# Performance work log

Measured on AMD Instinct MI355X. Metric: run time of the kernel, lower is better.

Reference implementation:

```python
import jax, jax.numpy as jnp
import numpy as np
import math

B, N, FEAT, H, NONGT, M, POS = 16, 1024, 768, 8, 20, 10, 64
DG = FEAT // H  # per-head dim = 96
NEG = -9e15


def setup_inputs() -> dict:
    key = jax.random.key(0)
    ks = jax.random.split(key, 14)
    s = 0.02
    return dict(
        roi_feat=jax.random.normal(ks[0], (B, N, FEAT), jnp.float32),
        adj_matrix=jax.random.randint(ks[1], (B, N, NONGT), 0, 2).astype(jnp.int32),
        position_embedding=jax.random.uniform(ks[2], (B, N, NONGT, POS), jnp.float32),
        label_biases_att=jax.random.normal(ks[3], (B, N, NONGT), jnp.float32) * 0.1,
        aux_feat=jax.random.normal(ks[4], (B, 1, FEAT), jnp.float32),
        Wq=jax.random.normal(ks[5], (FEAT, FEAT), jnp.float32) * s,
        bq=jnp.zeros((FEAT,), jnp.float32),
        Wk=jax.random.normal(ks[6], (FEAT, FEAT), jnp.float32) * s,
        bk=jnp.zeros((FEAT,), jnp.float32),
        Wpos=jax.random.normal(ks[7], (POS, H), jnp.float32) * s,
        bpos=jnp.zeros((H,), jnp.float32),
        m_k=jax.random.normal(ks[8], (1, M, FEAT), jnp.float32) * (1.0 / FEAT / H),
        m_v=jax.random.normal(ks[9], (1, M, FEAT), jnp.float32) * (1.0 / M),
        Wout=jax.random.normal(ks[10], (H, DG, FEAT), jnp.float32) * s,  # grouped 1x1 conv: per-head [DG, FEAT]
        bout=jnp.zeros((FEAT,), jnp.float32),
    )


def reference(roi_feat, adj_matrix, position_embedding, label_biases_att, aux_feat,
              Wq, bq, Wk, bk, Wpos, bpos, m_k, m_v, Wout, bout):
    b, n, f = roi_feat.shape
    nongt = min(NONGT, n)
    nongt_feat = roi_feat[:, :nongt]                               # [B,nongt,F]

    q = (roi_feat @ Wq + bq).reshape(b, n, H, DG)                  # [B,N,H,DG]
    scale_m = math.sqrt(f / H)
    mk = scale_m * m_k * aux_feat                                  # [B,M,F] (broadcast)
    mv = scale_m * m_v * aux_feat                                  # [B,M,F]
    k = jnp.concatenate([nongt_feat @ Wk + bk, mk], axis=1)        # [B,K,F], K=nongt+M
    v = jnp.concatenate([nongt_feat, mv], axis=1)                  # [B,K,F]
    kk = k.reshape(b, nongt + M, H, DG)

    # scaled QK^T -> [B,N,H,K]
    aff = jnp.einsum('bnhd,bkhd->bnhk', q, kk) / math.sqrt(DG)

    # geometric position bias: log(max(relu(fc(pos)), 1e-6)) on first nongt keys
    pos = jax.nn.relu(position_embedding @ Wpos + bpos)            # [B,N,nongt,H]
    bias = jnp.log(jnp.maximum(pos, 1e-6))
    aff_n = aff[:, :, :, :nongt] + jnp.transpose(bias, (0, 1, 3, 2))

    # adjacency mask + label bias on first nongt keys
    mask = (adj_matrix > 0)[:, :, None, :]                         # [B,N,1,nongt]
    aff_n = jnp.where(mask, aff_n, NEG) + label_biases_att[:, :, None, :]

    weighted = jnp.concatenate([aff_n, aff[:, :, :, nongt:]], axis=-1)
    p = jax.nn.softmax(weighted, axis=-1)                          # [B,N,H,K]

    out_t = jnp.einsum('bnhk,bkf->bnhf', p, v)                     # [B,N,H,F]
    # weight-normed grouped 1x1 conv == per-head linear F -> DG, concat over heads
    out = jnp.einsum('bnhf,hgf->bnhg', out_t, Wout).reshape(b, n, f) + bout
    return out
```

## Files before the change

kernel.cpp:

```cpp
#include <hip/hip_runtime.h>
#include <hip/hip_bf16.h>
#include <cstdint>

typedef __bf16 bf16;
typedef __bf16 bf16x4 __attribute__((ext_vector_type(4)));
typedef __bf16 bf16x8 __attribute__((ext_vector_type(8)));
typedef float f32x4 __attribute__((ext_vector_type(4)));

#define B_ 16
#define N_ 1024
#define FEAT_ 768
#define H_ 8
#define NONGT_ 20
#define M_ 10
#define POS_ 64
#define DG_ 96
#define KTOT_ 30
#define KPAD_ 32
#define ROWS_ (B_*N_)
#define SCALE_M 9.797958971132712f
#define INV_SQRT_DG 0.10206207261596575f
#define NEG_ -9.0e15f

__device__ __forceinline__ void gload16(const void* g, void* lds) {
  __builtin_amdgcn_global_load_lds(
      (const __attribute__((address_space(1))) unsigned int*)g,
      (__attribute__((address_space(3))) unsigned int*)lds, 16, 0, 0);
}

__device__ __forceinline__ bf16x8 cvt8(float4 a, float4 b) {
  bf16x8 o;
  o[0]=(bf16)a.x; o[1]=(bf16)a.y; o[2]=(bf16)a.z; o[3]=(bf16)a.w;
  o[4]=(bf16)b.x; o[5]=(bf16)b.y; o[6]=(bf16)b.z; o[7]=(bf16)b.w;
  return o;
}

__global__ void prep_kernel(const float* __restrict__ Wq, const float* __restrict__ Wk,
                            const float* __restrict__ Wout, const float* __restrict__ roi,
                            const float* __restrict__ aux, const float* __restrict__ m_v,
                            const float* __restrict__ m_k,
                            bf16* __restrict__ Wq_t, bf16* __restrict__ Wk_t,
                            bf16* __restrict__ Whi, bf16* __restrict__ Wlo,
                            bf16* __restrict__ Vbf, bf16* __restrict__ kbuf,
                            bf16* __restrict__ Abf)
{
  int idx = blockIdx.x * blockDim.x + threadIdx.x;
  int stride = gridDim.x * blockDim.x;
  for (int i = idx; i < FEAT_*FEAT_; i += stride) {
    int k = i / FEAT_, n = i % FEAT_;
    int ksw = (k & ~31) | (((((k >> 3) & 3) ^ ((n >> 1) & 3))) << 3) | (k & 7);
    Wq_t[(size_t)n*FEAT_ + ksw] = (bf16)Wq[i];
    Wk_t[(size_t)n*FEAT_ + k]   = (bf16)Wk[i];
    float w = Wout[i];
    bf16 hi = (bf16)w;
    Whi[i] = hi;
    Wlo[i] = (bf16)(w - (float)hi);
  }
  for (int i = idx; i < B_*KPAD_*FEAT_; i += stride) {
    int f = i % FEAT_;
    int r = (i / FEAT_) % KPAD_;
    int b = i / (FEAT_*KPAD_);
    float v;
    if (r < NONGT_)      v = roi[((size_t)b*N_ + r)*FEAT_ + f];
    else if (r < KTOT_)  v = SCALE_M * m_v[(r-NONGT_)*FEAT_ + f] * aux[b*FEAT_ + f];
    else                 v = 0.f;
    Vbf[i] = (bf16)v;
  }
  for (int i = idx; i < B_*12*FEAT_; i += stride) {
    int f = i % FEAT_;
    int rr = (i / FEAT_) % 12;
    int b = i / (FEAT_*12);
    float v = (rr < M_) ? SCALE_M * m_k[rr*FEAT_ + f] * aux[b*FEAT_ + f] : 0.f;
    kbuf[((size_t)b*KPAD_ + NONGT_ + rr)*FEAT_ + f] = (bf16)v;
  }
  const int total8 = ROWS_*FEAT_/8;
  for (int i = idx; i < total8; i += stride) {
    int row = i / (FEAT_/8);
    int col = (i % (FEAT_/8)) * 8;
    int slot_sw = ((col >> 3) & 3) ^ ((row >> 1) & 3);
    const float4* p = (const float4*)(roi + (size_t)i*8);
    *(bf16x8*)(Abf + (size_t)row*FEAT_ + (col & ~31) + slot_sw*8) = cvt8(p[0], p[1]);
  }
}

__global__ __launch_bounds__(256, 8) void posbias_kernel(
    const float* __restrict__ pe, const float* __restrict__ Wpos,
    const float* __restrict__ bpos, float* __restrict__ posb)
{
  __shared__ __align__(16) float sW[POS_*H_];
  __shared__ float sbp[H_];
  const int tid = threadIdx.x;
  sW[tid] = Wpos[tid];
  sW[256 + tid] = Wpos[256 + tid];
  if (tid < H_) sbp[tid] = bpos[tid];
  __syncthreads();
  const size_t g = (size_t)blockIdx.x*256 + tid;
  const float4* per = (const float4*)(pe + g*POS_);
  double acc[8];
  #pragma unroll
  for (int h = 0; h < 8; ++h) acc[h] = (double)sbp[h];
  #pragma unroll
  for (int p4 = 0; p4 < 16; ++p4) {
    float4 a = per[p4];
    float av[4] = {a.x, a.y, a.z, a.w};
    #pragma unroll
    for (int e = 0; e < 4; ++e) {
      const double ad = (double)av[e];
      const float* wp = sW + (p4*4 + e)*8;
      #pragma unroll
      for (int h = 0; h < 8; ++h)
        acc[h] = fma(ad, (double)wp[h], acc[h]);
    }
  }
  float o[8];
  #pragma unroll
  for (int h = 0; h < 8; ++h) {
    float x = (float)acc[h];
    o[h] = __logf(fmaxf(fmaxf(x, 0.f), 1e-6f));
  }
  float4* po = (float4*)(posb + g*8);
  po[0] = (float4){o[0], o[1], o[2], o[3]};
  po[1] = (float4){o[4], o[5], o[6], o[7]};
}

__global__ __launch_bounds__(256, 2) void gemm_fused_kernel(
    const bf16* __restrict__ Abf, const float* __restrict__ roi,
    const bf16* __restrict__ Wq_t,
    const float* __restrict__ bq, bf16* __restrict__ qbuf,
    const bf16* __restrict__ Wk_t, const bf16* __restrict__ Vbf,
    const bf16* __restrict__ Whi, const bf16* __restrict__ Wlo,
    const float* __restrict__ bk, bf16* __restrict__ kbuf,
    bf16* __restrict__ vwT_hi, bf16* __restrict__ vwT_lo)
{
  __shared__ __align__(16) bf16 sA[128*32];
  __shared__ __align__(16) bf16 sB[128*32];
  const int tid = threadIdx.x;
  const int w = tid >> 6, l = tid & 63;
  const int bx = blockIdx.x;
  const int fr = l & 15, fq = l >> 4, fko = fq << 3;

  if (bx < 768) {
    const int x = bx & 7, j = bx >> 3;
    const int mbase = (x + 8*(j/6)) * 128;
    const int nbase = (j % 6) * 128;
    const int wr = w >> 1, wc = w & 1;
    const int srow = tid >> 2;
    const int scol = (tid & 3) << 3;
    const bf16* Ag0 = Abf + (size_t)(mbase + srow)*FEAT_ + scol;
    const bf16* Ag1 = Ag0 + (size_t)64*FEAT_;
    const bf16* Bg0 = Wq_t + (size_t)(nbase + srow)*FEAT_ + scol;
    const bf16* Bg1 = Bg0 + (size_t)64*FEAT_;
    bf16* ldsA0 = sA + w*512;
    bf16* ldsA1 = sA + 2048 + w*512;
    bf16* ldsB0 = sB + w*512;
    bf16* ldsB1 = sB + 2048 + w*512;
    const int fko_sw = ((fq ^ ((fr >> 1) & 3)) << 3);
    f32x4 acc[4][4] = {};
    for (int kt = 0; kt < FEAT_/32; ++kt) {
      __syncthreads();
      gload16(Ag0 + kt*32, ldsA0);
      gload16(Ag1 + kt*32, ldsA1);
      gload16(Bg0 + kt*32, ldsB0);
      gload16(Bg1 + kt*32, ldsB1);
      __syncthreads();
      bf16x8 af[4], bff[4];
      #pragma unroll
      for (int m = 0; m < 4; ++m)
        af[m] = *(const bf16x8*)(sA + (wr*64 + m*16 + fr)*32 + fko_sw);
      #pragma unroll
      for (int n = 0; n < 4; ++n)
        bff[n] = *(const bf16x8*)(sB + (wc*64 + n*16 + fr)*32 + fko_sw);
      #pragma unroll
      for (int m = 0; m < 4; ++m) {
        #pragma unroll
        for (int n = 0; n < 4; ++n)
          acc[m][n] = __builtin_amdgcn_mfma_f32_16x16x32_bf16(af[m], bff[n], acc[m][n], 0, 0, 0);
      }
    }
    #pragma unroll
    for (int n = 0; n < 4; ++n) {
      const int col = nbase + wc*64 + n*16 + fr;
      const float bv = bq[col];
      #pragma unroll
      for (int m = 0; m < 4; ++m) {
        const int row = mbase + wr*64 + m*16 + fq*4;
        #pragma unroll
        for (int r = 0; r < 4; ++r)
          qbuf[(size_t)(row + r)*FEAT_ + col] = (bf16)(acc[m][n][r] + bv);
      }
    }
  } else {
    const int widx = (bx - 768)*4 + w;
    const int cbase = (widx % 48) * 16;
    const int by = widx / 48;
    f32x4 acc = {};
    if (by < 32) {
      const float* Ap = roi + ((size_t)(by >> 1)*N_ + (by & 1)*16 + fr)*FEAT_ + fko;
      const bf16* Bp = Wk_t + (size_t)(cbase + fr)*FEAT_ + fko;
      #pragma unroll
      for (int kt = 0; kt < FEAT_/32; ++kt) {
        float4 a0 = *(const float4*)(Ap + kt*32);
        float4 a1 = *(const float4*)(Ap + kt*32 + 4);
        bf16x8 b = *(const bf16x8*)(Bp + kt*32);
        acc = __builtin_amdgcn_mfma_f32_16x16x32_bf16(cvt8(a0, a1), b, acc, 0, 0, 0);
      }
      const float bv = bk[cbase + fr];
      #pragma unroll
      for (int r = 0; r < 4; ++r) {
        const int rl = (by & 1)*16 + fq*4 + r;
        if (rl < NONGT_)
          kbuf[((size_t)(by >> 1)*KPAD_ + rl)*FEAT_ + cbase + fr] = (bf16)(acc[r] + bv);
      }
    } else {
      const int rt = by - 32;
      const bf16* Ap = Vbf + ((size_t)rt*16 + fr)*FEAT_ + fko;
      const bf16* B1 = Whi + (size_t)(cbase + fr)*FEAT_ + fko;
      const bf16* B2 = Wlo + (size_t)(cbase + fr)*FEAT_ + fko;
      f32x4 acc2 = {};
      #pragma unroll
      for (int kt = 0; kt < FEAT_/32; ++kt) {
        bf16x8 a = *(const bf16x8*)(Ap + kt*32);
        acc  = __builtin_amdgcn_mfma_f32_16x16x32_bf16(a, *(const bf16x8*)(B1 + kt*32), acc,  0, 0, 0);
        acc2 = __builtin_amdgcn_mfma_f32_16x16x32_bf16(a, *(const bf16x8*)(B2 + kt*32), acc2, 0, 0, 0);
      }
      #pragma unroll
      for (int r = 0; r < 4; ++r) {
        const int grow = rt*16 + fq*4 + r;
        const int b = grow >> 5, key = grow & 31;
        float vv = acc[r] + acc2[r];
        bf16 vh = (bf16)vv;
        size_t addr = ((size_t)b*FEAT_ + cbase + fr)*KPAD_ + key;
        vwT_hi[addr] = vh;
        vwT_lo[addr] = (bf16)(vv - (float)vh);
      }
    }
  }
}

__global__ __launch_bounds__(256, 4) void attn_kernel(
    const bf16* __restrict__ qbuf, const bf16* __restrict__ kbuf,
    const bf16* __restrict__ vwT_hi, const bf16* __restrict__ vwT_lo,
    const float* __restrict__ posb, const int* __restrict__ adj,
    const float* __restrict__ lb, const float* __restrict__ bout,
    float* __restrict__ out)
{
  __shared__ __align__(16) bf16 sph[H_*16*40];
  __shared__ __align__(16) bf16 spl[H_*16*40];
  const int tid = threadIdx.x;
  const int w = tid >> 6, l = tid & 63;
  const int fr = l & 15, fq = l >> 4, fko = fq << 3;
  const int row0 = blockIdx.x * 16;
  const int b = blockIdx.y;
  const size_t rabs = (size_t)b*N_ + row0 + fr;

  #pragma unroll
  for (int hi2 = 0; hi2 < 2; ++hi2) {
    const int h = w*2 + hi2;
    const bf16* kp = kbuf + (size_t)b*KPAD_*FEAT_ + h*DG_ + fko;
    const bf16* qp = qbuf + rabs*FEAT_ + h*DG_ + fko;
    f32x4 acc0 = {}, acc1 = {};
    #pragma unroll
    for (int kt = 0; kt < 3; ++kt) {
      bf16x8 qa = *(const bf16x8*)(qp + kt*32);
      bf16x8 k0 = *(const bf16x8*)(kp + (size_t)fr*FEAT_ + kt*32);
      bf16x8 k1 = *(const bf16x8*)(kp + (size_t)(16 + fr)*FEAT_ + kt*32);
      acc0 = __builtin_amdgcn_mfma_f32_16x16x32_bf16(k0, qa, acc0, 0, 0, 0);
      acc1 = __builtin_amdgcn_mfma_f32_16x16x32_bf16(k1, qa, acc1, 0, 0, 0);
    }
    const float* pbr = posb + rabs*160;
    const int*   adjr = adj + rabs*20;
    const float* lbr  = lb  + rabs*20;
    float lg[2][4];
    #pragma unroll
    for (int r = 0; r < 4; ++r) {
      int j0 = fq*4 + r;
      float v0 = acc0[r] * INV_SQRT_DG;
      v0 = (adjr[j0] > 0 ? v0 + pbr[j0*8 + h] : NEG_) + lbr[j0];
      lg[0][r] = v0;
      int j1 = 16 + fq*4 + r;
      float v1 = acc1[r] * INV_SQRT_DG;
      if (j1 < NONGT_)      v1 = (adjr[j1] > 0 ? v1 + pbr[j1*8 + h] : NEG_) + lbr[j1];
      else if (j1 >= KTOT_) v1 = -3.0e38f;
      lg[1][r] = v1;
    }
    float m = lg[0][0];
    #pragma unroll
    for (int jt = 0; jt < 2; ++jt)
      #pragma unroll
      for (int r = 0; r < 4; ++r) m = fmaxf(m, lg[jt][r]);
    m = fmaxf(m, __shfl_xor(m, 16));
    m = fmaxf(m, __shfl_xor(m, 32));
    float s = 0.f;
    float e[2][4];
    #pragma unroll
    for (int jt = 0; jt < 2; ++jt)
      #pragma unroll
      for (int r = 0; r < 4; ++r) { e[jt][r] = __expf(lg[jt][r] - m); s += e[jt][r]; }
    s += __shfl_xor(s, 16);
    s += __shfl_xor(s, 32);
    const float inv = 1.f / s;
    #pragma unroll
    for (int jt = 0; jt < 2; ++jt) {
      bf16x4 ph, pl;
      #pragma unroll
      for (int r = 0; r < 4; ++r) {
        float p = e[jt][r] * inv;
        ph[r] = (bf16)p;
        pl[r] = (bf16)(p - (float)ph[r]);
      }
      const int off = (h*16 + fr)*40 + jt*16 + fq*4;
      *(bf16x4*)(sph + off) = ph;
      *(bf16x4*)(spl + off) = pl;
    }
    bf16x8 pa_h = *(const bf16x8*)(sph + (h*16 + fr)*40 + fko);
    bf16x8 pa_l = *(const bf16x8*)(spl + (h*16 + fr)*40 + fko);
    #pragma unroll
    for (int ct = 0; ct < 6; ++ct) {
      const int col = h*DG_ + ct*16 + fr;
      const size_t vaddr = ((size_t)b*FEAT_ + col)*KPAD_ + fko;
      bf16x8 vh = *(const bf16x8*)(vwT_hi + vaddr);
      bf16x8 vl = *(const bf16x8*)(vwT_lo + vaddr);
      f32x4 o = {};
      o = __builtin_amdgcn_mfma_f32_16x16x32_bf16(pa_h, vh, o, 0, 0, 0);
      o = __builtin_amdgcn_mfma_f32_16x16x32_bf16(pa_h, vl, o, 0, 0, 0);
      o = __builtin_amdgcn_mfma_f32_16x16x32_bf16(pa_l, vh, o, 0, 0, 0);
      const float bv = bout[col];
      #pragma unroll
      for (int r = 0; r < 4; ++r)
        out[((size_t)b*N_ + row0 + fq*4 + r)*FEAT_ + col] = o[r] + bv;
    }
  }
}

extern "C" void kernel_launch(void* const* d_in, const int* in_sizes, int n_in,
                              void* d_out, int out_size, void* d_ws, size_t ws_size,
                              hipStream_t stream) {
  const float* roi  = (const float*)d_in[0];
  const int*   adj  = (const int*)  d_in[1];
  const float* pe   = (const float*)d_in[2];
  const float* lb   = (const float*)d_in[3];
  const float* aux  = (const float*)d_in[4];
  const float* Wq   = (const float*)d_in[5];
  const float* bq   = (const float*)d_in[6];
  const float* Wk   = (const float*)d_in[7];
  const float* bk   = (const float*)d_in[8];
  const float* Wpos = (const float*)d_in[9];
  const float* bpos = (const float*)d_in[10];
  const float* m_k  = (const float*)d_in[11];
  const float* m_v  = (const float*)d_in[12];
  const float* Wout = (const float*)d_in[13];
  const float* bout = (const float*)d_in[14];
  float* out = (float*)d_out;

  char* pw = (char*)d_ws;
  auto carve = [&](size_t bytes) -> void* {
    void* r = pw; pw += (bytes + 255) & ~(size_t)255; return r;
  };
  bf16*  Abf    = (bf16*) carve((size_t)ROWS_*FEAT_*2);
  bf16*  qbuf   = (bf16*) carve((size_t)ROWS_*FEAT_*2);
  bf16*  Wq_t   = (bf16*) carve((size_t)FEAT_*FEAT_*2);
  bf16*  Wk_t   = (bf16*) carve((size_t)FEAT_*FEAT_*2);
  bf16*  Whi    = (bf16*) carve((size_t)FEAT_*FEAT_*2);
  bf16*  Wlo    = (bf16*) carve((size_t)FEAT_*FEAT_*2);
  bf16*  Vbf    = (bf16*) carve((size_t)B_*KPAD_*FEAT_*2);
  bf16*  kbuf   = (bf16*) carve((size_t)B_*KPAD_*FEAT_*2);
  bf16*  vwT_hi = (bf16*) carve((size_t)B_*FEAT_*KPAD_*2);
  bf16*  vwT_lo = (bf16*) carve((size_t)B_*FEAT_*KPAD_*2);
  float* posb   = (float*)carve((size_t)ROWS_*160*4);

  posbias_kernel<<<dim3(ROWS_*NONGT_/256), dim3(256), 0, stream>>>(pe, Wpos, bpos, posb);
  prep_kernel<<<dim3(2048), dim3(256), 0, stream>>>(Wq, Wk, Wout, roi, aux, m_v, m_k,
                                                    Wq_t, Wk_t, Whi, Wlo, Vbf, kbuf, Abf);
  gemm_fused_kernel<<<dim3(1536), dim3(256), 0, stream>>>(Abf, roi, Wq_t, bq, qbuf,
                                                          Wk_t, Vbf, Whi, Wlo, bk, kbuf,
                                                          vwT_hi, vwT_lo);
  attn_kernel<<<dim3(64, 16), dim3(256), 0, stream>>>(qbuf, kbuf, vwT_hi, vwT_lo,
                                                      posb, adj, lb, bout, out);
}
```

Measured before the change: 134.0 us.

## Merge posbias into fused GEMM kernel and double K-step per LDS stage

Folds the position-bias kernel into the fused Q/K/V GEMM launch, interleaving GEMM tiles, small K/V-projection warps and posbias blocks within each group of block indices. This removes one launch and lets the memory-bound posbias work overlap the compute-bound GEMM. The Q GEMM now stages 64 K-columns per iteration in a larger LDS buffer, halving the barrier count. The cost is higher LDS use per block (32KB), which may reduce occupancy for every block type.

```diff
diff --git a/kernel.cpp b/kernel.cpp
--- a/kernel.cpp
+++ b/kernel.cpp
@@ -83,66 +83,29 @@
   }
 }
 
-__global__ __launch_bounds__(256, 8) void posbias_kernel(
-    const float* __restrict__ pe, const float* __restrict__ Wpos,
-    const float* __restrict__ bpos, float* __restrict__ posb)
-{
-  __shared__ __align__(16) float sW[POS_*H_];
-  __shared__ float sbp[H_];
-  const int tid = threadIdx.x;
-  sW[tid] = Wpos[tid];
-  sW[256 + tid] = Wpos[256 + tid];
-  if (tid < H_) sbp[tid] = bpos[tid];
-  __syncthreads();
-  const size_t g = (size_t)blockIdx.x*256 + tid;
-  const float4* per = (const float4*)(pe + g*POS_);
-  double acc[8];
-  #pragma unroll
-  for (int h = 0; h < 8; ++h) acc[h] = (double)sbp[h];
-  #pragma unroll
-  for (int p4 = 0; p4 < 16; ++p4) {
-    float4 a = per[p4];
-    float av[4] = {a.x, a.y, a.z, a.w};
-    #pragma unroll
-    for (int e = 0; e < 4; ++e) {
-      const double ad = (double)av[e];
-      const float* wp = sW + (p4*4 + e)*8;
-      #pragma unroll
-      for (int h = 0; h < 8; ++h)
-        acc[h] = fma(ad, (double)wp[h], acc[h]);
-    }
-  }
-  float o[8];
-  #pragma unroll
-  for (int h = 0; h < 8; ++h) {
-    float x = (float)acc[h];
-    o[h] = __logf(fmaxf(fmaxf(x, 0.f), 1e-6f));
-  }
-  float4* po = (float4*)(posb + g*8);
-  po[0] = (float4){o[0], o[1], o[2], o[3]};
-  po[1] = (float4){o[4], o[5], o[6], o[7]};
-}
-
-__global__ __launch_bounds__(256, 2) void gemm_fused_kernel(
+__global__ __launch_bounds__(256, 2) void mid_kernel(
     const bf16* __restrict__ Abf, const float* __restrict__ roi,
     const bf16* __restrict__ Wq_t,
     const float* __restrict__ bq, bf16* __restrict__ qbuf,
     const bf16* __restrict__ Wk_t, const bf16* __restrict__ Vbf,
     const bf16* __restrict__ Whi, const bf16* __restrict__ Wlo,
     const float* __restrict__ bk, bf16* __restrict__ kbuf,
-    bf16* __restrict__ vwT_hi, bf16* __restrict__ vwT_lo)
+    bf16* __restrict__ vwT_hi, bf16* __restrict__ vwT_lo,
+    const float* __restrict__ pe, const float* __restrict__ Wpos,
+    const float* __restrict__ bpos, float* __restrict__ posb)
 {
-  __shared__ __align__(16) bf16 sA[128*32];
-  __shared__ __align__(16) bf16 sB[128*32];
+  __shared__ __align__(16) bf16 smem[16384];
   const int tid = threadIdx.x;
   const int w = tid >> 6, l = tid & 63;
-  const int bx = blockIdx.x;
+  const int x = blockIdx.x & 7, j = blockIdx.x >> 3;
+  const int g = j / 22, r = j % 22;
   const int fr = l & 15, fq = l >> 4, fko = fq << 3;
 
-  if (bx < 768) {
-    const int x = bx & 7, j = bx >> 3;
-    const int mbase = (x + 8*(j/6)) * 128;
-    const int nbase = (j % 6) * 128;
+  if (r < 6) {
+    bf16* sA = smem;
+    bf16* sB = smem + 8192;
+    const int mbase = (x + 8*g) * 128;
+    const int nbase = r * 128;
     const int wr = w >> 1, wc = w & 1;
     const int srow = tid >> 2;
     const int scol = (tid & 3) << 3;
@@ -150,32 +113,40 @@
     const bf16* Ag1 = Ag0 + (size_t)64*FEAT_;
     const bf16* Bg0 = Wq_t + (size_t)(nbase + srow)*FEAT_ + scol;
     const bf16* Bg1 = Bg0 + (size_t)64*FEAT_;
-    bf16* ldsA0 = sA + w*512;
-    bf16* ldsA1 = sA + 2048 + w*512;
-    bf16* ldsB0 = sB + w*512;
-    bf16* ldsB1 = sB + 2048 + w*512;
     const int fko_sw = ((fq ^ ((fr >> 1) & 3)) << 3);
     f32x4 acc[4][4] = {};
-    for (int kt = 0; kt < FEAT_/32; ++kt) {
+    gload16(Bg0, sB + w*512);          gload16(Bg1, sB + 2048 + w*512);
+    gload16(Bg0 + 32, sB + 4096 + w*512); gload16(Bg1 + 32, sB + 6144 + w*512);
+    gload16(Ag0, sA + w*512);          gload16(Ag1, sA + 2048 + w*512);
+    gload16(Ag0 + 32, sA + 4096 + w*512); gload16(Ag1 + 32, sA + 6144 + w*512);
+    __syncthreads();
+    for (int t = 0; t < 12; ++t) {
+      #pragma unroll
+      for (int half = 0; half < 2; ++half) {
+        const int bo = half * 4096;
+        bf16x8 af[4], bff[4];
+        #pragma unroll
+        for (int m = 0; m < 4; ++m)
+          af[m] = *(const bf16x8*)(sA + bo + (wr*64 + m*16 + fr)*32 + fko_sw);
+        #pragma unroll
+        for (int n = 0; n < 4; ++n)
+          bff[n] = *(const bf16x8*)(sB + bo + (wc*64 + n*16 + fr)*32 + fko_sw);
+        #pragma unroll
+        for (int m = 0; m < 4; ++m) {
+          #pragma unroll
+          for (int n = 0; n < 4; ++n)
+            acc[m][n] = __builtin_amdgcn_mfma_f32_16x16x32_bf16(af[m], bff[n], acc[m][n], 0, 0, 0);
+        }
+      }
       __syncthreads();
-      gload16(Ag0 + kt*32, ldsA0);
-      gload16(Ag1 + kt*32, ldsA1);
-      gload16(Bg0 + kt*32, ldsB0);
-      gload16(Bg1 + kt*32, ldsB1);
+      if (t < 11) {
+        const int ko = (t + 1) * 64;
+        gload16(Bg0 + ko, sB + w*512);           gload16(Bg1 + ko, sB + 2048 + w*512);
+        gload16(Bg0 + ko + 32, sB + 4096 + w*512); gload16(Bg1 + ko + 32, sB + 6144 + w*512);
+        gload16(Ag0 + ko, sA + w*512);           gload16(Ag1 + ko, sA + 2048 + w*512);
+        gload16(Ag0 + ko + 32, sA + 4096 + w*512); gload16(Ag1 + ko + 32, sA + 6144 + w*512);
+      }
       __syncthreads();
-      bf16x8 af[4], bff[4];
-      #pragma unroll
-      for (int m = 0; m < 4; ++m)
-        af[m] = *(const bf16x8*)(sA + (wr*64 + m*16 + fr)*32 + fko_sw);
-      #pragma unroll
-      for (int n = 0; n < 4; ++n)
-        bff[n] = *(const bf16x8*)(sB + (wc*64 + n*16 + fr)*32 + fko_sw);
-      #pragma unroll
-      for (int m = 0; m < 4; ++m) {
-        #pragma unroll
-        for (int n = 0; n < 4; ++n)
-          acc[m][n] = __builtin_amdgcn_mfma_f32_16x16x32_bf16(af[m], bff[n], acc[m][n], 0, 0, 0);
-      }
     }
     #pragma unroll
     for (int n = 0; n < 4; ++n) {
@@ -185,12 +156,12 @@
       for (int m = 0; m < 4; ++m) {
         const int row = mbase + wr*64 + m*16 + fq*4;
         #pragma unroll
-        for (int r = 0; r < 4; ++r)
-          qbuf[(size_t)(row + r)*FEAT_ + col] = (bf16)(acc[m][n][r] + bv);
-      }
-    }
-  } else {
-    const int widx = (bx - 768)*4 + w;
+        for (int rr = 0; rr < 4; ++rr)
+          qbuf[(size_t)(row + rr)*FEAT_ + col] = (bf16)(acc[m][n][rr] + bv);
+      }
+    }
+  } else if (r < 12) {
+    const int widx = (x*96 + g*6 + (r - 6))*4 + w;
     const int cbase = (widx % 48) * 16;
     const int by = widx / 48;
     f32x4 acc = {};
@@ -206,10 +177,10 @@
       }
       const float bv = bk[cbase + fr];
       #pragma unroll
-      for (int r = 0; r < 4; ++r) {
-        const int rl = (by & 1)*16 + fq*4 + r;
+      for (int rr = 0; rr < 4; ++rr) {
+        const int rl = (by & 1)*16 + fq*4 + rr;
         if (rl < NONGT_)
-          kbuf[((size_t)(by >> 1)*KPAD_ + rl)*FEAT_ + cbase + fr] = (bf16)(acc[r] + bv);
+          kbuf[((size_t)(by >> 1)*KPAD_ + rl)*FEAT_ + cbase + fr] = (bf16)(acc[rr] + bv);
       }
     } else {
       const int rt = by - 32;
@@ -224,16 +195,51 @@
         acc2 = __builtin_amdgcn_mfma_f32_16x16x32_bf16(a, *(const bf16x8*)(B2 + kt*32), acc2, 0, 0, 0);
       }
       #pragma unroll
-      for (int r = 0; r < 4; ++r) {
-        const int grow = rt*16 + fq*4 + r;
+      for (int rr = 0; rr < 4; ++rr) {
+        const int grow = rt*16 + fq*4 + rr;
         const int b = grow >> 5, key = grow & 31;
-        float vv = acc[r] + acc2[r];
+        float vv = acc[rr] + acc2[rr];
         bf16 vh = (bf16)vv;
         size_t addr = ((size_t)b*FEAT_ + cbase + fr)*KPAD_ + key;
         vwT_hi[addr] = vh;
         vwT_lo[addr] = (bf16)(vv - (float)vh);
       }
     }
+  } else {
+    float* sW = (float*)smem;
+    float* sbp = (float*)smem + 512;
+    sW[tid] = Wpos[tid];
+    sW[256 + tid] = Wpos[256 + tid];
+    if (tid < H_) sbp[tid] = bpos[tid];
+    __syncthreads();
+    const int pb = x*160 + g*10 + (r - 12);
+    const size_t gg = (size_t)pb*256 + tid;
+    const float4* per = (const float4*)(pe + gg*POS_);
+    double acc[8];
+    #pragma unroll
+    for (int h = 0; h < 8; ++h) acc[h] = (double)sbp[h];
+    #pragma unroll
+    for (int p4 = 0; p4 < 16; ++p4) {
+      float4 a = per[p4];
+      float av[4] = {a.x, a.y, a.z, a.w};
+      #pragma unroll
+      for (int e = 0; e < 4; ++e) {
+        const double ad = (double)av[e];
+        const float* wp = sW + (p4*4 + e)*8;
+        #pragma unroll
+        for (int h = 0; h < 8; ++h)
+          acc[h] = fma(ad, (double)wp[h], acc[h]);
+      }
+    }
+    float o[8];
+    #pragma unroll
+    for (int h = 0; h < 8; ++h) {
+      float xx = (float)acc[h];
+      o[h] = __logf(fmaxf(fmaxf(xx, 0.f), 1e-6f));
+    }
+    float4* po = (float4*)(posb + gg*8);
+    po[0] = (float4){o[0], o[1], o[2], o[3]};
+    po[1] = (float4){o[4], o[5], o[6], o[7]};
   }
 }
 
@@ -368,12 +374,12 @@
   bf16*  vwT_lo = (bf16*) carve((size_t)B_*FEAT_*KPAD_*2);
   float* posb   = (float*)carve((size_t)ROWS_*160*4);
 
-  posbias_kernel<<<dim3(ROWS_*NONGT_/256), dim3(256), 0, stream>>>(pe, Wpos, bpos, posb);
   prep_kernel<<<dim3(2048), dim3(256), 0, stream>>>(Wq, Wk, Wout, roi, aux, m_v, m_k,
                                                     Wq_t, Wk_t, Whi, Wlo, Vbf, kbuf, Abf);
-  gemm_fused_kernel<<<dim3(1536), dim3(256), 0, stream>>>(Abf, roi, Wq_t, bq, qbuf,
-                                                          Wk_t, Vbf, Whi, Wlo, bk, kbuf,
-                                                          vwT_hi, vwT_lo);
+  mid_kernel<<<dim3(2816), dim3(256), 0, stream>>>(Abf, roi, Wq_t, bq, qbuf,
+                                                   Wk_t, Vbf, Whi, Wlo, bk, kbuf,
+                                                   vwT_hi, vwT_lo,
+                                                   pe, Wpos, bpos, posb);
   attn_kernel<<<dim3(64, 16), dim3(256), 0, stream>>>(qbuf, kbuf, vwT_hi, vwT_lo,
                                                       posb, adj, lb, bout, out);
 }
```

Result: faster. 128.2 us (-4.3%).
